# Kernel optimization log

Measured on AMD Instinct MI355X. Metric: run time of the kernel, lower is better.

Reference implementation:

```python
import jax, jax.numpy as jnp
import numpy as np

DIM, HEADS = 384, 8

def conv2d(x, w, groups=1):
    return jax.lax.conv_general_dilated(
        x, w, window_strides=(1, 1), padding='SAME',
        dimension_numbers=('NCHW', 'OIHW', 'NCHW'),
        feature_group_count=groups)

def l2norm(x, eps=1e-12):
    n = jnp.sqrt(jnp.sum(x * x, axis=-1, keepdims=True))
    return x / jnp.maximum(n, eps)

def setup_inputs() -> dict:
    key = jax.random.key(0)
    ks = jax.random.split(key, 8)
    b, h, w = 4, 128, 128
    s = 0.05
    return {
        'x': jax.random.normal(ks[0], (b, DIM, h, w), jnp.float32),
        'mask': jax.random.randint(ks[1], (1, HEADS, DIM // HEADS, DIM // HEADS), 0, 2, jnp.int32),
        'qkv_w': jax.random.normal(ks[2], (3 * DIM, DIM, 1, 1), jnp.float32) * s,
        'dw_w': jax.random.normal(ks[3], (3 * DIM, 1, 3, 3), jnp.float32) * s,
        'proj_w': jax.random.normal(ks[4], (DIM, DIM, 1, 1), jnp.float32) * s,
        'temperature': jnp.ones((HEADS, 1, 1), jnp.float32),
        'w_blend': jnp.ones((2,), jnp.float32),
        'pos_w1': jax.random.normal(ks[5], (DIM, 1, 3, 3), jnp.float32) * s,
        'pos_w2': jax.random.normal(ks[6], (DIM, 1, 3, 3), jnp.float32) * s,
    }

def reference(x, mask, qkv_w, dw_w, proj_w, temperature, w_blend, pos_w1, pos_w2):
    b, c, h, w = x.shape
    cph = c // HEADS  # channels per head
    qkv = conv2d(conv2d(x, qkv_w), dw_w, groups=3 * c)
    q, k, v_pos = jnp.split(qkv, 3, axis=1)
    def to_heads(t):
        return t.reshape(b, HEADS, cph, h * w)
    q = l2norm(to_heads(q))
    k = l2norm(to_heads(k))
    v = to_heads(v_pos)
    # channel-wise attention: (b, head, c, c)
    attn0 = jnp.einsum('bhcn,bhdn->bhcd', q, k) * temperature
    attn1 = jnp.where(mask == 0, jnp.float32(-1e9), attn0)
    wsm = jax.nn.softmax(w_blend)
    attn = jax.nn.softmax(attn0, axis=-1) * wsm[0] + jax.nn.softmax(attn1, axis=-1) * wsm[1]
    out = jnp.einsum('bhcd,bhdn->bhcn', attn, v).reshape(b, c, h, w)
    out = conv2d(out, proj_w)
    pos = conv2d(jax.nn.gelu(conv2d(v_pos, pos_w1, groups=c), approximate=False), pos_w2, groups=c)
    return pos + out
```

## Files before the change

kernel.cpp:

```cpp
#include <hip/hip_runtime.h>
#include <math.h>

#define CDIM 384
#define C3   1152
#define HH   128
#define WW   128
#define NPIX 16384
#define NHEADS 8
#define CPH  48

typedef short bf16x8 __attribute__((ext_vector_type(8)));
typedef float f32x4  __attribute__((ext_vector_type(4)));
typedef unsigned short u16x8 __attribute__((ext_vector_type(8)));

__device__ __forceinline__ float bf2f(unsigned short h) {
    union { unsigned u; float f; } x; x.u = ((unsigned)h) << 16; return x.f;
}
__device__ __forceinline__ unsigned short f2bf(float f) {
    union { float f; unsigned u; } x; x.f = f;
    unsigned r = x.u + 0x7fffu + ((x.u >> 16) & 1u);
    return (unsigned short)(r >> 16);
}

#define ASYNC_CP16(gp, lp) \
    __builtin_amdgcn_global_load_lds( \
        (const __attribute__((address_space(1))) unsigned int*)(gp), \
        (__attribute__((address_space(3))) unsigned int*)(lp), 16, 0, 0)

__global__ __launch_bounds__(256) void cast_bf16_kernel(
    const float* __restrict__ in, unsigned short* __restrict__ out, int n4)
{
    int i = blockIdx.x * 256 + threadIdx.x;
    if (i < n4) {
        float4 v = *(const float4*)(in + (size_t)i * 4);
        ushort4 o = { f2bf(v.x), f2bf(v.y), f2bf(v.z), f2bf(v.w) };
        *(ushort4*)(out + (size_t)i * 4) = o;
    }
}

template<int IN_BF16>
__global__ __launch_bounds__(256) void transpose_kernel(
    const void* __restrict__ in_, unsigned short* __restrict__ out, size_t in_zstride)
{
    const int z = blockIdx.z;
    const int n0 = blockIdx.x * 64, k0 = blockIdx.y * 64;
    __shared__ unsigned short tile[64][69];
    const int t = threadIdx.x;
    if (IN_BF16) {
        const unsigned short* in = (const unsigned short*)in_ + (size_t)z * in_zstride;
        #pragma unroll
        for (int r = 0; r < 4; ++r) {
            int kk = r * 16 + (t >> 4), nn = (t & 15) * 4;
            ushort4 v = *(const ushort4*)(in + (size_t)(k0 + kk) * NPIX + n0 + nn);
            tile[kk][nn] = v.x; tile[kk][nn + 1] = v.y;
            tile[kk][nn + 2] = v.z; tile[kk][nn + 3] = v.w;
        }
    } else {
        const float* in = (const float*)in_ + (size_t)z * in_zstride;
        #pragma unroll
        for (int r = 0; r < 4; ++r) {
            int kk = r * 16 + (t >> 4), nn = (t & 15) * 4;
            float4 v = *(const float4*)(in + (size_t)(k0 + kk) * NPIX + n0 + nn);
            tile[kk][nn] = f2bf(v.x); tile[kk][nn + 1] = f2bf(v.y);
            tile[kk][nn + 2] = f2bf(v.z); tile[kk][nn + 3] = f2bf(v.w);
        }
    }
    __syncthreads();
    unsigned short* o = out + (size_t)z * NPIX * CDIM;
    #pragma unroll
    for (int r = 0; r < 2; ++r) {
        int nn = r * 32 + (t >> 3), kk = (t & 7) * 8;
        ushort4 a, b;
        a.x = tile[kk + 0][nn]; a.y = tile[kk + 1][nn];
        a.z = tile[kk + 2][nn]; a.w = tile[kk + 3][nn];
        b.x = tile[kk + 4][nn]; b.y = tile[kk + 5][nn];
        b.z = tile[kk + 6][nn]; b.w = tile[kk + 7][nn];
        *(ushort4*)(o + (size_t)(n0 + nn) * CDIM + k0 + kk) = a;
        *(ushort4*)(o + (size_t)(n0 + nn) * CDIM + k0 + kk + 4) = b;
    }
}

template<int OUT_BF16, int A_PER_Z>
__global__ __launch_bounds__(256) void mfma_gemm_kernel(
    const unsigned short* __restrict__ A, const unsigned short* __restrict__ Bt,
    void* __restrict__ C, int M)
{
    const int z = blockIdx.z;
    const int n0 = blockIdx.x * 128;
    const int m0 = blockIdx.y * 128;
    const unsigned short* a = A + (A_PER_Z ? (size_t)z * M * CDIM : 0);
    const unsigned short* bt = Bt + (size_t)z * NPIX * CDIM;
    const int t = threadIdx.x;
    const int wave = t >> 6, lane = t & 63;
    const int wm = (wave & 1) * 64, wn = (wave >> 1) * 64;
    const int lm = lane & 15, lq = lane >> 4;

    __shared__ unsigned short a_s[128 * 32];
    __shared__ unsigned short b_s[128 * 32];

    f32x4 acc[4][4];
    #pragma unroll
    for (int i = 0; i < 4; ++i)
        #pragma unroll
        for (int j = 0; j < 4; ++j)
            acc[i][j] = (f32x4){0.f, 0.f, 0.f, 0.f};

    const int srow = t >> 2, scol = (t & 3) * 8;

    for (int k0 = 0; k0 < CDIM; k0 += 32) {
        #pragma unroll
        for (int r = 0; r < 2; ++r)
            ASYNC_CP16(a + (size_t)(m0 + r * 64 + srow) * CDIM + k0 + scol,
                       a_s + (r * 64 + srow) * 32 + scol);
        #pragma unroll
        for (int r = 0; r < 2; ++r)
            ASYNC_CP16(bt + (size_t)(n0 + r * 64 + srow) * CDIM + k0 + scol,
                       b_s + (r * 64 + srow) * 32 + scol);
        __syncthreads();
        bf16x8 af[4], bfr[4];
        #pragma unroll
        for (int i = 0; i < 4; ++i)
            af[i] = *(const bf16x8*)(a_s + (wm + i * 16 + lm) * 32 + lq * 8);
        #pragma unroll
        for (int j = 0; j < 4; ++j)
            bfr[j] = *(const bf16x8*)(b_s + (wn + j * 16 + lm) * 32 + lq * 8);
        #pragma unroll
        for (int i = 0; i < 4; ++i)
            #pragma unroll
            for (int j = 0; j < 4; ++j)
                acc[i][j] = __builtin_amdgcn_mfma_f32_16x16x32_bf16(
                    af[i], bfr[j], acc[i][j], 0, 0, 0);
        __syncthreads();
    }

    if (OUT_BF16) {
        unsigned short* c = (unsigned short*)C + (size_t)z * M * NPIX;
        #pragma unroll
        for (int i = 0; i < 4; ++i)
            #pragma unroll
            for (int j = 0; j < 4; ++j) {
                size_t base = (size_t)(m0 + wm + i * 16 + lq * 4) * NPIX
                            + (n0 + wn + j * 16 + lm);
                #pragma unroll
                for (int r = 0; r < 4; ++r)
                    c[base + (size_t)r * NPIX] = f2bf(acc[i][j][r]);
            }
    } else {
        float* c = (float*)C + (size_t)z * M * NPIX;
        #pragma unroll
        for (int i = 0; i < 4; ++i)
            #pragma unroll
            for (int j = 0; j < 4; ++j) {
                size_t base = (size_t)(m0 + wm + i * 16 + lq * 4) * NPIX
                            + (n0 + wn + j * 16 + lm);
                #pragma unroll
                for (int r = 0; r < 4; ++r)
                    c[base + (size_t)r * NPIX] = acc[i][j][r];
            }
    }
}

__device__ __forceinline__ void row10_bf(const unsigned short* row, int x0, float* a)
{
    u16x8 v = *(const u16x8*)(row + x0);
    a[0] = (x0 == 0) ? 0.f : bf2f(row[x0 - 1]);
    #pragma unroll
    for (int i = 0; i < 8; ++i) a[1 + i] = bf2f((unsigned short)v[i]);
    a[9] = (x0 == 120) ? 0.f : bf2f(row[x0 + 8]);
}

__global__ __launch_bounds__(256) void dwconv_fast_kernel(
    const unsigned short* __restrict__ X, const float* __restrict__ Wd,
    unsigned short* __restrict__ Y, float* __restrict__ norms2)
{
    const int z = blockIdx.z, c = blockIdx.y, s0 = blockIdx.x * 32;
    const int t = threadIdx.x;
    const unsigned short* xin = X + ((size_t)z * C3 + c) * NPIX;
    __shared__ unsigned short xs[34 * 136];

    for (int g = t; g < 34 * 16; g += 256) {
        const int r = g >> 4, cg = (g & 15) << 3;
        const int y = s0 - 1 + r;
        u16x8 v = (u16x8)(short)0;
        if (y >= 0 && y < HH) v = *(const u16x8*)(xin + y * WW + cg);
        *(u16x8*)(xs + r * 136 + cg) = v;
    }
    __syncthreads();

    float w[9];
    #pragma unroll
    for (int i = 0; i < 9; ++i) w[i] = Wd[c * 9 + i];

    const int r0 = (t >> 4) * 2, x0 = (t & 15) * 8;
    const bool do_ss = (c < 2 * CDIM);
    float ss = 0.f;
    #pragma unroll
    for (int orow = 0; orow < 2; ++orow) {
        const int ry = r0 + orow;
        float a0[10], a1[10], a2[10];
        row10_bf(xs + (ry + 0) * 136, x0, a0);
        row10_bf(xs + (ry + 1) * 136, x0, a1);
        row10_bf(xs + (ry + 2) * 136, x0, a2);
        unsigned short ob[8];
        #pragma unroll
        for (int px = 0; px < 8; ++px) {
            float s = w[0] * a0[px] + w[1] * a0[px + 1] + w[2] * a0[px + 2]
                    + w[3] * a1[px] + w[4] * a1[px + 1] + w[5] * a1[px + 2]
                    + w[6] * a2[px] + w[7] * a2[px + 1] + w[8] * a2[px + 2];
            if (do_ss) ss += s * s;
            ob[px] = f2bf(s);
        }
        *(uint4*)(Y + ((size_t)z * C3 + c) * NPIX + (s0 + ry) * WW + x0) = *(uint4*)ob;
    }

    if (do_ss) {
        #pragma unroll
        for (int off = 32; off; off >>= 1) ss += __shfl_xor(ss, off, 64);
        __shared__ float red[4];
        if ((t & 63) == 0) red[t >> 6] = ss;
        __syncthreads();
        if (t == 0) {
            const int qk = c / CDIM, ch = c % CDIM;
            atomicAdd(&norms2[((size_t)z * 2 + qk) * CDIM + ch],
                      red[0] + red[1] + red[2] + red[3]);
        }
    }
}

__global__ __launch_bounds__(256) void pos_fused_kernel(
    const unsigned short* __restrict__ QKdw, const float* __restrict__ W1,
    const float* __restrict__ W2, float* __restrict__ Out)
{
    const int z = blockIdx.z, c = blockIdx.y, s0 = blockIdx.x * 32;
    const int t = threadIdx.x;
    const unsigned short* vin = QKdw + ((size_t)z * C3 + 2 * CDIM + c) * NPIX;
    __shared__ unsigned short vs[36 * 136];
    __shared__ float ts[34 * 132];

    for (int g = t; g < 36 * 16; g += 256) {
        const int r = g >> 4, cg = (g & 15) << 3;
        const int y = s0 - 2 + r;
        u16x8 v = (u16x8)(short)0;
        if (y >= 0 && y < HH) v = *(const u16x8*)(vin + y * WW + cg);
        *(u16x8*)(vs + r * 136 + cg) = v;
    }
    __syncthreads();

    float w1[9], w2[9];
    #pragma unroll
    for (int i = 0; i < 9; ++i) { w1[i] = W1[c * 9 + i]; w2[i] = W2[c * 9 + i]; }

    const int r0 = (t >> 4) * 2, x0 = (t & 15) * 8;

    #pragma unroll
    for (int orow = 0; orow < 2; ++orow) {
        const int tr = 1 + r0 + orow;
        float a0[10], a1[10], a2[10];
        row10_bf(vs + (tr + 0) * 136, x0, a0);
        row10_bf(vs + (tr + 1) * 136, x0, a1);
        row10_bf(vs + (tr + 2) * 136, x0, a2);
        #pragma unroll
        for (int px = 0; px < 8; ++px) {
            float s = w1[0] * a0[px] + w1[1] * a0[px + 1] + w1[2] * a0[px + 2]
                    + w1[3] * a1[px] + w1[4] * a1[px + 1] + w1[5] * a1[px + 2]
                    + w1[6] * a2[px] + w1[7] * a2[px + 1] + w1[8] * a2[px + 2];
            ts[tr * 132 + x0 + px] = 0.5f * s * (1.0f + erff(s * 0.70710678118654752f));
        }
    }
    if (t < 32) {
        const int tr = (t >> 4) ? 33 : 0;
        const int xh = (t & 15) * 8;
        const int yt = s0 - 1 + tr;
        if (yt < 0 || yt >= HH) {
            #pragma unroll
            for (int px = 0; px < 8; ++px) ts[tr * 132 + xh + px] = 0.f;
        } else {
            float a0[10], a1[10], a2[10];
            row10_bf(vs + (tr + 0) * 136, xh, a0);
            row10_bf(vs + (tr + 1) * 136, xh, a1);
            row10_bf(vs + (tr + 2) * 136, xh, a2);
            #pragma unroll
            for (int px = 0; px < 8; ++px) {
                float s = w1[0] * a0[px] + w1[1] * a0[px + 1] + w1[2] * a0[px + 2]
                        + w1[3] * a1[px] + w1[4] * a1[px + 1] + w1[5] * a1[px + 2]
                        + w1[6] * a2[px] + w1[7] * a2[px + 1] + w1[8] * a2[px + 2];
                ts[tr * 132 + xh + px] = 0.5f * s * (1.0f + erff(s * 0.70710678118654752f));
            }
        }
    }
    __syncthreads();

    float* ob = Out + ((size_t)z * CDIM + c) * NPIX;
    #pragma unroll
    for (int orow = 0; orow < 2; ++orow) {
        const int o = r0 + orow;
        float b0[10], b1[10], b2[10];
        #pragma unroll
        for (int rr = 0; rr < 3; ++rr) {
            float* dst = (rr == 0) ? b0 : (rr == 1) ? b1 : b2;
            const float* trow = ts + (o + rr) * 132;
            float4 v0 = *(const float4*)(trow + x0);
            float4 v1 = *(const float4*)(trow + x0 + 4);
            dst[0] = (x0 == 0) ? 0.f : trow[x0 - 1];
            dst[1] = v0.x; dst[2] = v0.y; dst[3] = v0.z; dst[4] = v0.w;
            dst[5] = v1.x; dst[6] = v1.y; dst[7] = v1.z; dst[8] = v1.w;
            dst[9] = (x0 == 120) ? 0.f : trow[x0 + 8];
        }
        float res[8];
        #pragma unroll
        for (int px = 0; px < 8; ++px)
            res[px] = w2[0] * b0[px] + w2[1] * b0[px + 1] + w2[2] * b0[px + 2]
                    + w2[3] * b1[px] + w2[4] * b1[px + 1] + w2[5] * b1[px + 2]
                    + w2[6] * b2[px] + w2[7] * b2[px + 1] + w2[8] * b2[px + 2];
        float* op = ob + (s0 + o) * WW + x0;
        float4 c0 = *(const float4*)op, c1 = *(const float4*)(op + 4);
        c0.x += res[0]; c0.y += res[1]; c0.z += res[2]; c0.w += res[3];
        c1.x += res[4]; c1.y += res[5]; c1.z += res[6]; c1.w += res[7];
        *(float4*)op = c0; *(float4*)(op + 4) = c1;
    }
}

__global__ __launch_bounds__(256) void scores_mfma_kernel(
    const unsigned short* __restrict__ QKdw, float* __restrict__ S)
{
    const int z = blockIdx.z, h = blockIdx.y, chunk = blockIdx.x;
    const unsigned short* qb = QKdw + ((size_t)z * C3 + h * CPH) * NPIX;
    const unsigned short* kb = qb + (size_t)CDIM * NPIX;
    const int t = threadIdx.x, wave = t >> 6, lane = t & 63;
    const int lm = lane & 15, lq = lane >> 4;
    const int kw0 = chunk * 2048 + wave * 512;

    f32x4 acc[3][3];
    #pragma unroll
    for (int i = 0; i < 3; ++i)
        #pragma unroll
        for (int j = 0; j < 3; ++j)
            acc[i][j] = (f32x4){0.f, 0.f, 0.f, 0.f};

    for (int ks = 0; ks < 512; ks += 32) {
        const int kk = kw0 + ks + lq * 8;
        bf16x8 af[3], bfr[3];
        #pragma unroll
        for (int i = 0; i < 3; ++i)
            af[i] = *(const bf16x8*)(qb + (size_t)(i * 16 + lm) * NPIX + kk);
        #pragma unroll
        for (int j = 0; j < 3; ++j)
            bfr[j] = *(const bf16x8*)(kb + (size_t)(j * 16 + lm) * NPIX + kk);
        #pragma unroll
        for (int i = 0; i < 3; ++i)
            #pragma unroll
            for (int j = 0; j < 3; ++j)
                acc[i][j] = __builtin_amdgcn_mfma_f32_16x16x32_bf16(
                    af[i], bfr[j], acc[i][j], 0, 0, 0);
    }
    __shared__ float s_red[CPH * CPH];
    for (int e = t; e < CPH * CPH; e += 256) s_red[e] = 0.f;
    __syncthreads();
    #pragma unroll
    for (int i = 0; i < 3; ++i)
        #pragma unroll
        for (int j = 0; j < 3; ++j)
            #pragma unroll
            for (int r = 0; r < 4; ++r)
                atomicAdd(&s_red[(i * 16 + lq * 4 + r) * CPH + j * 16 + lm], acc[i][j][r]);
    __syncthreads();
    float* Sb = S + (size_t)(z * NHEADS + h) * CPH * CPH;
    for (int e = t; e < CPH * CPH; e += 256) atomicAdd(&Sb[e], s_red[e]);
}

__global__ __launch_bounds__(64) void softmax_kernel(
    float* __restrict__ S, const float* __restrict__ norms2,
    const int* __restrict__ mask, const float* __restrict__ temp,
    const float* __restrict__ wblend)
{
    const int z = blockIdx.z, h = blockIdx.y, c = blockIdx.x;
    const int d = threadIdx.x;
    float* Srow = S + ((size_t)(z * NHEADS + h) * CPH + c) * CPH;
    const float nq = fmaxf(sqrtf(norms2[((size_t)z * 2 + 0) * CDIM + h * CPH + c]), 1e-12f);
    float a0 = -INFINITY, a1 = -INFINITY;
    if (d < CPH) {
        const float nk = fmaxf(sqrtf(norms2[((size_t)z * 2 + 1) * CDIM + h * CPH + d]), 1e-12f);
        a0 = Srow[d] / (nq * nk) * temp[h];
        a1 = (mask[(h * CPH + c) * CPH + d] == 0) ? -1e9f : a0;
    }
    float m0 = a0, m1 = a1;
    #pragma unroll
    for (int off = 32; off; off >>= 1) {
        m0 = fmaxf(m0, __shfl_xor(m0, off, 64));
        m1 = fmaxf(m1, __shfl_xor(m1, off, 64));
    }
    float e0 = (d < CPH) ? expf(a0 - m0) : 0.f;
    float e1 = (d < CPH) ? expf(a1 - m1) : 0.f;
    float s0 = e0, s1 = e1;
    #pragma unroll
    for (int off = 32; off; off >>= 1) {
        s0 += __shfl_xor(s0, off, 64);
        s1 += __shfl_xor(s1, off, 64);
    }
    const float b0 = wblend[0], b1 = wblend[1];
    const float bm = fmaxf(b0, b1);
    const float eb0 = expf(b0 - bm), eb1 = expf(b1 - bm);
    const float ws0 = eb0 / (eb0 + eb1), ws1 = eb1 / (eb0 + eb1);
    if (d < CPH) Srow[d] = (e0 / s0) * ws0 + (e1 / s1) * ws1;
}

__global__ __launch_bounds__(256) void mproj_kernel(
    const float* __restrict__ S, const float* __restrict__ P,
    unsigned short* __restrict__ Mcat)
{
    const int z = blockIdx.y, h = blockIdx.x;
    __shared__ float As[CPH * CPH];
    const float* Sb = S + (size_t)(z * NHEADS + h) * CPH * CPH;
    for (int e = threadIdx.x; e < CPH * CPH; e += 256) As[e] = Sb[e];
    __syncthreads();
    unsigned short* Mz = Mcat + (size_t)z * CDIM * CDIM;
    for (int e = threadIdx.x; e < CDIM * CPH; e += 256) {
        const int m = e / CPH, d = e % CPH;
        const float* pr = P + (size_t)m * CDIM + h * CPH;
        float s = 0.f;
        #pragma unroll
        for (int c = 0; c < CPH; ++c) s = fmaf(pr[c], As[c * CPH + d], s);
        Mz[(size_t)m * CDIM + h * CPH + d] = f2bf(s);
    }
}

extern "C" void kernel_launch(void* const* d_in, const int* in_sizes, int n_in,
                              void* d_out, int out_size, void* d_ws, size_t ws_size,
                              hipStream_t stream)
{
    const float* x      = (const float*)d_in[0];
    const int*   mask   = (const int*)d_in[1];
    const float* qkv_w  = (const float*)d_in[2];
    const float* dw_w   = (const float*)d_in[3];
    const float* proj_w = (const float*)d_in[4];
    const float* temp   = (const float*)d_in[5];
    const float* wblend = (const float*)d_in[6];
    const float* pos_w1 = (const float*)d_in[7];
    const float* pos_w2 = (const float*)d_in[8];
    float* out = (float*)d_out;

    auto need = [](size_t nb) {
        return nb * ((size_t)NPIX * CDIM * 2
                   + (size_t)C3 * NPIX * 2
                   + (size_t)C3 * NPIX * 2
                   + (size_t)NHEADS * CPH * CPH * 4
                   + (size_t)2 * CDIM * 4
                   + (size_t)CDIM * CDIM * 2)
             + (size_t)C3 * CDIM * 2;
    };
    int nb = 4;
    if (need(4) > ws_size) nb = (need(2) <= ws_size) ? 2 : 1;

    char* p = (char*)d_ws;
    unsigned short* w_bf  = (unsigned short*)p; p += (size_t)C3 * CDIM * 2;
    unsigned short* x_t   = (unsigned short*)p; p += (size_t)nb * NPIX * CDIM * 2;
    unsigned short* qkv0  = (unsigned short*)p; p += (size_t)nb * C3 * NPIX * 2;
    unsigned short* qkvdw = (unsigned short*)p; p += (size_t)nb * C3 * NPIX * 2;
    float* S      = (float*)p; p += (size_t)nb * NHEADS * CPH * CPH * 4;
    float* norms2 = (float*)p; p += (size_t)nb * 2 * CDIM * 4;
    unsigned short* Mcat = (unsigned short*)p;
    unsigned short* v_t = qkv0;

    cast_bf16_kernel<<<dim3(C3 * CDIM / 4 / 256), 256, 0, stream>>>(qkv_w, w_bf, C3 * CDIM / 4);

    for (int b0 = 0; b0 < 4; b0 += nb) {
        const float* xb = x + (size_t)b0 * CDIM * NPIX;
        float* outb = out + (size_t)b0 * CDIM * NPIX;

        hipMemsetAsync(S, 0, (size_t)nb * NHEADS * CPH * CPH * 4, stream);
        hipMemsetAsync(norms2, 0, (size_t)nb * 2 * CDIM * 4, stream);

        transpose_kernel<0><<<dim3(NPIX / 64, CDIM / 64, nb), 256, 0, stream>>>(
            xb, x_t, (size_t)CDIM * NPIX);
        mfma_gemm_kernel<1, 0><<<dim3(NPIX / 128, C3 / 128, nb), 256, 0, stream>>>(
            w_bf, x_t, qkv0, C3);
        dwconv_fast_kernel<<<dim3(4, C3, nb), 256, 0, stream>>>(
            qkv0, dw_w, qkvdw, norms2);
        scores_mfma_kernel<<<dim3(8, NHEADS, nb), 256, 0, stream>>>(qkvdw, S);
        softmax_kernel<<<dim3(CPH, NHEADS, nb), 64, 0, stream>>>(
            S, norms2, mask, temp, wblend);
        mproj_kernel<<<dim3(NHEADS, nb), 256, 0, stream>>>(S, proj_w, Mcat);
        transpose_kernel<1><<<dim3(NPIX / 64, CDIM / 64, nb), 256, 0, stream>>>(
            qkvdw + (size_t)2 * CDIM * NPIX, v_t, (size_t)C3 * NPIX);
        mfma_gemm_kernel<0, 1><<<dim3(NPIX / 128, CDIM / 128, nb), 256, 0, stream>>>(
            Mcat, v_t, outb, CDIM);
        pos_fused_kernel<<<dim3(4, CDIM, nb), 256, 0, stream>>>(
            qkvdw, pos_w1, pos_w2, outb);
    }
}
```

Baseline: 575.8 us.

## Swizzle GEMM LDS tiles and route attention output through fp16 scratch

The GEMM now XOR-swizzles the k-chunk positions in its LDS tiles, so the MFMA fragment reads hit fewer bank conflicts. The attention-output GEMM writes an fp16 intermediate into the reused x_t buffer instead of fp32 into the output. The pos kernel then reads that fp16 value and writes the final sum directly, dropping the fp32 read-modify-write of the output. The cost is reduced precision in the attention branch, since it is rounded to fp16 before the add.

```diff
diff --git a/kernel.cpp b/kernel.cpp
--- a/kernel.cpp
+++ b/kernel.cpp
@@ -12,6 +12,7 @@
 typedef short bf16x8 __attribute__((ext_vector_type(8)));
 typedef float f32x4  __attribute__((ext_vector_type(4)));
 typedef unsigned short u16x8 __attribute__((ext_vector_type(8)));
+typedef _Float16 f16x8 __attribute__((ext_vector_type(8)));
 
 __device__ __forceinline__ float bf2f(unsigned short h) {
     union { unsigned u; float f; } x; x.u = ((unsigned)h) << 16; return x.f;
@@ -80,7 +81,7 @@
     }
 }
 
-template<int OUT_BF16, int A_PER_Z>
+template<int OUT_MODE, int A_PER_Z>
 __global__ __launch_bounds__(256) void mfma_gemm_kernel(
     const unsigned short* __restrict__ A, const unsigned short* __restrict__ Bt,
     void* __restrict__ C, int M)
@@ -105,25 +106,29 @@
         for (int j = 0; j < 4; ++j)
             acc[i][j] = (f32x4){0.f, 0.f, 0.f, 0.f};
 
-    const int srow = t >> 2, scol = (t & 3) * 8;
+    const int srow = t >> 2;
+    const int kbs  = ((t & 3) ^ ((t >> 3) & 3)) * 8;
+    const int sdst = (t & 3) * 8;
+    const int rsw  = ((lm >> 1) & 3);
 
     for (int k0 = 0; k0 < CDIM; k0 += 32) {
         #pragma unroll
         for (int r = 0; r < 2; ++r)
-            ASYNC_CP16(a + (size_t)(m0 + r * 64 + srow) * CDIM + k0 + scol,
-                       a_s + (r * 64 + srow) * 32 + scol);
+            ASYNC_CP16(a + (size_t)(m0 + r * 64 + srow) * CDIM + k0 + kbs,
+                       a_s + (r * 64 + srow) * 32 + sdst);
         #pragma unroll
         for (int r = 0; r < 2; ++r)
-            ASYNC_CP16(bt + (size_t)(n0 + r * 64 + srow) * CDIM + k0 + scol,
-                       b_s + (r * 64 + srow) * 32 + scol);
+            ASYNC_CP16(bt + (size_t)(n0 + r * 64 + srow) * CDIM + k0 + kbs,
+                       b_s + (r * 64 + srow) * 32 + sdst);
         __syncthreads();
         bf16x8 af[4], bfr[4];
+        const int ko = (lq ^ rsw) * 8;
         #pragma unroll
         for (int i = 0; i < 4; ++i)
-            af[i] = *(const bf16x8*)(a_s + (wm + i * 16 + lm) * 32 + lq * 8);
+            af[i] = *(const bf16x8*)(a_s + (wm + i * 16 + lm) * 32 + ko);
         #pragma unroll
         for (int j = 0; j < 4; ++j)
-            bfr[j] = *(const bf16x8*)(b_s + (wn + j * 16 + lm) * 32 + lq * 8);
+            bfr[j] = *(const bf16x8*)(b_s + (wn + j * 16 + lm) * 32 + ko);
         #pragma unroll
         for (int i = 0; i < 4; ++i)
             #pragma unroll
@@ -133,7 +138,7 @@
         __syncthreads();
     }
 
-    if (OUT_BF16) {
+    if (OUT_MODE == 1) {
         unsigned short* c = (unsigned short*)C + (size_t)z * M * NPIX;
         #pragma unroll
         for (int i = 0; i < 4; ++i)
@@ -144,6 +149,18 @@
                 #pragma unroll
                 for (int r = 0; r < 4; ++r)
                     c[base + (size_t)r * NPIX] = f2bf(acc[i][j][r]);
+            }
+    } else if (OUT_MODE == 2) {
+        _Float16* c = (_Float16*)C + (size_t)z * M * NPIX;
+        #pragma unroll
+        for (int i = 0; i < 4; ++i)
+            #pragma unroll
+            for (int j = 0; j < 4; ++j) {
+                size_t base = (size_t)(m0 + wm + i * 16 + lq * 4) * NPIX
+                            + (n0 + wn + j * 16 + lm);
+                #pragma unroll
+                for (int r = 0; r < 4; ++r)
+                    c[base + (size_t)r * NPIX] = (_Float16)acc[i][j][r];
             }
     } else {
         float* c = (float*)C + (size_t)z * M * NPIX;
@@ -228,8 +245,9 @@
 }
 
 __global__ __launch_bounds__(256) void pos_fused_kernel(
-    const unsigned short* __restrict__ QKdw, const float* __restrict__ W1,
-    const float* __restrict__ W2, float* __restrict__ Out)
+    const unsigned short* __restrict__ QKdw, const _Float16* __restrict__ Attn,
+    const float* __restrict__ W1, const float* __restrict__ W2,
+    float* __restrict__ Out)
 {
     const int z = blockIdx.z, c = blockIdx.y, s0 = blockIdx.x * 32;
     const int t = threadIdx.x;
@@ -291,6 +309,7 @@
     __syncthreads();
 
     float* ob = Out + ((size_t)z * CDIM + c) * NPIX;
+    const _Float16* ab = Attn + ((size_t)z * CDIM + c) * NPIX;
     #pragma unroll
     for (int orow = 0; orow < 2; ++orow) {
         const int o = r0 + orow;
@@ -306,17 +325,17 @@
             dst[5] = v1.x; dst[6] = v1.y; dst[7] = v1.z; dst[8] = v1.w;
             dst[9] = (x0 == 120) ? 0.f : trow[x0 + 8];
         }
+        f16x8 av = *(const f16x8*)(ab + (s0 + o) * WW + x0);
         float res[8];
         #pragma unroll
         for (int px = 0; px < 8; ++px)
-            res[px] = w2[0] * b0[px] + w2[1] * b0[px + 1] + w2[2] * b0[px + 2]
+            res[px] = (float)av[px]
+                    + w2[0] * b0[px] + w2[1] * b0[px + 1] + w2[2] * b0[px + 2]
                     + w2[3] * b1[px] + w2[4] * b1[px + 1] + w2[5] * b1[px + 2]
                     + w2[6] * b2[px] + w2[7] * b2[px + 1] + w2[8] * b2[px + 2];
         float* op = ob + (s0 + o) * WW + x0;
-        float4 c0 = *(const float4*)op, c1 = *(const float4*)(op + 4);
-        c0.x += res[0]; c0.y += res[1]; c0.z += res[2]; c0.w += res[3];
-        c1.x += res[4]; c1.y += res[5]; c1.z += res[6]; c1.w += res[7];
-        *(float4*)op = c0; *(float4*)(op + 4) = c1;
+        *(float4*)op = make_float4(res[0], res[1], res[2], res[3]);
+        *(float4*)(op + 4) = make_float4(res[4], res[5], res[6], res[7]);
     }
 }
 
@@ -460,6 +479,7 @@
     float* norms2 = (float*)p; p += (size_t)nb * 2 * CDIM * 4;
     unsigned short* Mcat = (unsigned short*)p;
     unsigned short* v_t = qkv0;
+    _Float16* attn_h = (_Float16*)x_t;
 
     cast_bf16_kernel<<<dim3(C3 * CDIM / 4 / 256), 256, 0, stream>>>(qkv_w, w_bf, C3 * CDIM / 4);
 
@@ -482,9 +502,9 @@
         mproj_kernel<<<dim3(NHEADS, nb), 256, 0, stream>>>(S, proj_w, Mcat);
         transpose_kernel<1><<<dim3(NPIX / 64, CDIM / 64, nb), 256, 0, stream>>>(
             qkvdw + (size_t)2 * CDIM * NPIX, v_t, (size_t)C3 * NPIX);
-        mfma_gemm_kernel<0, 1><<<dim3(NPIX / 128, CDIM / 128, nb), 256, 0, stream>>>(
-            Mcat, v_t, outb, CDIM);
+        mfma_gemm_kernel<2, 1><<<dim3(NPIX / 128, CDIM / 128, nb), 256, 0, stream>>>(
+            Mcat, v_t, attn_h, CDIM);
         pos_fused_kernel<<<dim3(4, CDIM, nb), 256, 0, stream>>>(
-            qkvdw, pos_w1, pos_w2, outb);
-    }
-}
+            qkvdw, attn_h, pos_w1, pos_w2, outb);
+    }
+}
```

After: 571.2 us. Within noise of the previous version (-0.8%).
